# Kernel optimization log

Measured on AMD Instinct MI355X. Metric: run time of the kernel, lower is better.

The kernel has to match this reference:

```python
import jax, jax.numpy as jnp
import numpy as np

# Model constants (match init_kwargs)
H, C, OV = 6, 64, 4          # in_freq, in_dim, overlap
G, NVQ = 3, 6                # num_pvqs, num_rvqs
K, D = 1024, 8               # codebook_size, codebook_dim
FIX = H * C                  # 384
GD = (FIX * OV) // G         # 512 per product group
EPS = 1e-12


def setup_inputs() -> dict:
    key = jax.random.key(0)
    k1, k2, k3, k4 = jax.random.split(key, 4)
    B, W = 32, 2400
    z_e = jax.random.normal(k1, (B, H * W, C), dtype=jnp.float32)
    proj_down = jax.random.normal(k2, (G, D, GD), dtype=jnp.float32) * 0.05   # Linear(GD->D), torch weight layout (out,in)
    proj_up = jax.random.normal(k3, (G, GD, D), dtype=jnp.float32) * 0.05     # Linear(D->GD)
    codebooks = jax.random.normal(k4, (G, NVQ, K, D), dtype=jnp.float32)      # kaiming-normal-ish init
    return {"z_e": z_e, "proj_down": proj_down, "proj_up": proj_up,
            "codebooks": codebooks, "num_streams": 6}


def _l2norm(x):
    return x / jnp.maximum(jnp.linalg.norm(x, axis=-1, keepdims=True), EPS)


def reference(z_e, proj_down, proj_up, codebooks, num_streams):
    B = z_e.shape[0]
    W = z_e.shape[1] // H
    T = W // OV
    # pre_process: b (h w) c -> b w (c h), then fold overlap frames
    z = z_e.reshape(B, H, W, C).transpose(0, 2, 3, 1).reshape(B, W, C * H)
    z = z.reshape(B, T, OV * FIX)
    # split into G contiguous groups of GD dims -> (G, B, T, GD)
    zg = z.reshape(B, T, G, GD).transpose(2, 0, 1, 3)

    def group_fn(x, pd, pu, cbs):
        zd = jnp.einsum('btg,dg->btd', x, pd)            # proj_down: (B,T,D)
        residual = zd
        zq = jnp.zeros_like(zd)
        codes = []
        cm = jnp.float32(0.0)
        cb = jnp.float32(0.0)
        for i in range(int(num_streams)):
            en = _l2norm(cbs[i])                          # (K,D) normalized codebook
            zn = _l2norm(residual)                        # (B,T,D)
            sim = jnp.einsum('btd,kd->btk', zn, en)       # cosine sim; argmax == argmin of L2 dist
            code = jnp.argmax(sim, axis=-1)               # (B,T)
            q = en[code]                                  # gather quantized vectors
            cm = cm + jnp.mean((residual - jax.lax.stop_gradient(q)) ** 2)
            cb = cb + jnp.mean((jax.lax.stop_gradient(residual) - q) ** 2)
            q_st = residual + jax.lax.stop_gradient(q - residual)  # straight-through
            residual = residual - q_st
            zq = zq + q_st
            codes.append(code)
        idx = jnp.stack(codes, axis=1)                    # (B,NVQ,T)
        up = jnp.einsum('btd,gd->btg', zq, pu)            # proj_up: (B,T,GD)
        return up, idx, cm, cb

    up, idx, cm, cb = jax.vmap(group_fn)(zg, proj_down, proj_up, codebooks)
    # merge groups: (G,B,T,GD) -> (B,T,G*GD)
    zq = up.transpose(1, 2, 0, 3).reshape(B, T, G * GD)
    indices = idx.transpose(1, 2, 0, 3)                   # (B,NVQ,G,T)
    cm_loss = jnp.mean(cm)                                # sum over groups / num groups
    cb_loss = jnp.mean(cb)
    # post_process: unfold overlap, then b w (c h) -> b (h w) c
    zq = zq.reshape(B, T, OV, FIX).reshape(B, W, FIX)
    zq = zq.reshape(B, W, C, H).transpose(0, 3, 1, 2).reshape(B, H * W, C)
    return zq, indices, cm_loss, cb_loss
```

## Files before the change

kernel.cpp:

```cpp
#include <hip/hip_runtime.h>
#include <cfloat>
#include <math.h>

constexpr int H_  = 6;
constexpr int C_  = 64;
constexpr int OV_ = 4;
constexpr int G_  = 3;
constexpr int NVQ_ = 6;
constexpr int K_  = 1024;
constexpr int D_  = 8;
constexpr int B_  = 32;
constexpr int W_  = 2400;
constexpr int T_  = 600;
constexpr int NPOS_ = B_ * T_;
constexpr int FIX_ = H_ * C_;
constexpr int GD_ = 512;

constexpr size_t OUT_ZQ   = 0;
constexpr size_t OUT_IDX  = (size_t)B_ * H_ * W_ * C_;
constexpr size_t OUT_LOSS = OUT_IDX + (size_t)B_ * NVQ_ * G_ * T_;

constexpr size_t WS_EN   = 0;
constexpr size_t WS_ZD   = WS_EN + (size_t)G_*NVQ_*K_*D_*8;
constexpr size_t WS_LOSS = WS_ZD + (size_t)G_*NPOS_*D_*8;
constexpr size_t WS_ZQ   = WS_LOSS + 64;


__global__ __launch_bounds__(256) void k1_norm_cb(const float* __restrict__ cb,
                                                  double* __restrict__ en,
                                                  float* __restrict__ en32,
                                                  double* __restrict__ loss) {
    int tid = blockIdx.x * 256 + threadIdx.x;
    if (tid == 0) loss[0] = 0.0;
    if (tid >= G_ * NVQ_ * K_) return;
    int k  = tid & (K_ - 1);
    int gi = tid >> 10;
    const float* row = cb + ((size_t)gi * K_ + k) * D_;
    double v[D_];
    double ss = 0.0;
#pragma unroll
    for (int d = 0; d < D_; d++) { v[d] = (double)row[d]; ss += v[d] * v[d]; }
    double n = sqrt(ss);
    if (n < 1e-12) n = 1e-12;
    double* dst64 = en + ((size_t)gi * K_ + k) * D_;
    float*  dst32 = en32 + ((size_t)gi * K_ + k) * D_;
#pragma unroll
    for (int d = 0; d < D_; d++) {
        double q = v[d] / n;
        dst64[d] = q;
        dst32[d] = (float)q;
    }
}

constexpr int PSTR_ = 1548;
constexpr int OVS_  = 388;

__global__ __launch_bounds__(256) void k2_fold_pd(const float* __restrict__ ze,
                                                  const float* __restrict__ pd,
                                                  double* __restrict__ zd) {
    __shared__ __align__(16) float zf[8 * PSTR_];
    int tid  = threadIdx.x;
    int pos0 = blockIdx.x * 8;
#pragma unroll
    for (int it = 0; it < 12; it++) {
        int slot = it * 256 + tid;
        int seg  = slot >> 6;
        int li   = slot & 63;
        int p = seg / 6, h = seg - p * 6;
        int pos = pos0 + p;
        int b = pos / T_, t = pos - b * T_;
        const float4 vv = *(const float4*)(ze + ((size_t)((b * H_ + h) * W_ + 4 * t)) * C_ + li * 4);
        int ov = li >> 4;
        int c0 = (li & 15) * 4;
        int base = p * PSTR_ + ov * OVS_ + h;
        zf[base + (c0 + 0) * 6] = vv.x;
        zf[base + (c0 + 1) * 6] = vv.y;
        zf[base + (c0 + 2) * 6] = vv.z;
        zf[base + (c0 + 3) * 6] = vv.w;
    }
    __syncthreads();
    if (tid < 192) {
        int p = tid / 24;
        int combo = tid - p * 24;
        int g = combo >> 3, d = combo & 7;
        const float* pdp = pd + ((size_t)g * D_ + d) * GD_;
        int lbase = p * PSTR_;
        double acc[4] = {0.0, 0.0, 0.0, 0.0};
        for (int jj = 0; jj < GD_; jj += 16) {
#pragma unroll
            for (int u = 0; u < 4; u++) {
                int j4  = jj + u * 4;
                int gd  = g * GD_ + j4;
                int ov  = gd / FIX_;
                int rem = gd - ov * FIX_;
                float4 zv = *(const float4*)&zf[lbase + ov * OVS_ + rem];
                float4 pv = *(const float4*)&pdp[j4];
                acc[u] = fma((double)pv.x, (double)zv.x, acc[u]);
                acc[u] = fma((double)pv.y, (double)zv.y, acc[u]);
                acc[u] = fma((double)pv.z, (double)zv.z, acc[u]);
                acc[u] = fma((double)pv.w, (double)zv.w, acc[u]);
            }
        }
        zd[((size_t)g * NPOS_ + pos0 + p) * D_ + d] = (acc[0] + acc[1]) + (acc[2] + acc[3]);
    }
}

__device__ __forceinline__ void screen1(const float4 lo, const float4 hi,
                                        const float r[8], int kk,
                                        float& smax, float& s2, int& sidx) {
    float s = lo.x * r[0];
    s = fmaf(lo.y, r[1], s);
    s = fmaf(lo.z, r[2], s);
    s = fmaf(lo.w, r[3], s);
    s = fmaf(hi.x, r[4], s);
    s = fmaf(hi.y, r[5], s);
    s = fmaf(hi.z, r[6], s);
    s = fmaf(hi.w, r[7], s);
    float l = fminf(s, smax);
    s2 = fmaxf(s2, l);
    if (s > smax) { smax = s; sidx = kk; }
}

__global__ __launch_bounds__(256) void k3_rvq(const double* __restrict__ en64,
                                              const float*  __restrict__ en32,
                                              const double* __restrict__ zd,
                                              float* __restrict__ zq,
                                              double* __restrict__ loss,
                                              float* __restrict__ out_idx) {
    __shared__ float smL[2][4][64];
    __shared__ float s2L[2][4][64];
    __shared__ int   idL[2][4][64];
    int tid  = threadIdx.x;
    int lane = tid & 63;
    int wu   = __builtin_amdgcn_readfirstlane(tid >> 6);
    int g     = blockIdx.x / 300;
    int chunk = blockIdx.x - g * 300;
    int pos   = chunk * 64 + lane;
    size_t zdbase = ((size_t)g * NPOS_ + pos) * D_;

    const double* en64g = en64 + (size_t)g * NVQ_ * K_ * D_;
    const float*  en32g = en32 + (size_t)g * NVQ_ * K_ * D_;

    double r64[8]; float r32[8];
    {
        const double* zp = zd + zdbase;
#pragma unroll
        for (int d = 0; d < 8; d++) { r64[d] = zp[d]; r32[d] = (float)r64[d]; }
    }
    double loss_acc = 0.0;

    for (int i = 0; i < NVQ_; i++) {
        int p = i & 1;
        int kb = wu * 256;
        const float* cp = en32g + ((size_t)i * K_ + kb) * D_;
        float smax = -FLT_MAX, s2 = -FLT_MAX; int sidx = 0;
        for (int c = 0; c < 256; c += 8) {
            const float4* q0 = (const float4*)(cp + (size_t)(c + 0) * 8);
            const float4* q1 = (const float4*)(cp + (size_t)(c + 1) * 8);
            const float4* q2 = (const float4*)(cp + (size_t)(c + 2) * 8);
            const float4* q3 = (const float4*)(cp + (size_t)(c + 3) * 8);
            const float4* q4 = (const float4*)(cp + (size_t)(c + 4) * 8);
            const float4* q5 = (const float4*)(cp + (size_t)(c + 5) * 8);
            const float4* q6 = (const float4*)(cp + (size_t)(c + 6) * 8);
            const float4* q7 = (const float4*)(cp + (size_t)(c + 7) * 8);
            float4 a0 = q0[0], b0 = q0[1];
            float4 a1 = q1[0], b1 = q1[1];
            float4 a2 = q2[0], b2 = q2[1];
            float4 a3 = q3[0], b3 = q3[1];
            float4 a4 = q4[0], b4 = q4[1];
            float4 a5 = q5[0], b5 = q5[1];
            float4 a6 = q6[0], b6 = q6[1];
            float4 a7 = q7[0], b7 = q7[1];
            screen1(a0, b0, r32, kb + c + 0, smax, s2, sidx);
            screen1(a1, b1, r32, kb + c + 1, smax, s2, sidx);
            screen1(a2, b2, r32, kb + c + 2, smax, s2, sidx);
            screen1(a3, b3, r32, kb + c + 3, smax, s2, sidx);
            screen1(a4, b4, r32, kb + c + 4, smax, s2, sidx);
            screen1(a5, b5, r32, kb + c + 5, smax, s2, sidx);
            screen1(a6, b6, r32, kb + c + 6, smax, s2, sidx);
            screen1(a7, b7, r32, kb + c + 7, smax, s2, sidx);
        }
        smL[p][wu][lane] = smax;
        s2L[p][wu][lane] = s2;
        idL[p][wu][lane] = sidx;
        __syncthreads();
        float sm  = smL[p][0][lane];
        float s2m = s2L[p][0][lane];
        int   si  = idL[p][0][lane];
#pragma unroll
        for (int w = 1; w < 4; w++) {
            float a  = smL[p][w][lane];
            float a2 = s2L[p][w][lane];
            int   ai = idL[p][w][lane];
            float l  = fminf(a, sm);
            s2m = fmaxf(s2m, fmaxf(l, a2));
            if (a > sm) { sm = a; si = ai; }
        }
        float rr = 0.f;
#pragma unroll
        for (int d = 0; d < 8; d++) rr = fmaf(r32[d], r32[d], rr);
        float gap = sm - s2m;
        bool need = !(gap * gap > 1.6e-11f * rr);
        if (__any(need)) {
            const double* bp = en64g + (size_t)i * K_ * D_;
            double bmax = -DBL_MAX; int bidx = 0;
            for (int k = 0; k < K_; k++) {
                const double* cq = bp + (size_t)k * 8;
                double sA = cq[0] * r64[0];
                double sB = cq[1] * r64[1];
                sA = fma(cq[2], r64[2], sA);
                sB = fma(cq[3], r64[3], sB);
                sA = fma(cq[4], r64[4], sA);
                sB = fma(cq[5], r64[5], sB);
                sA = fma(cq[6], r64[6], sA);
                sB = fma(cq[7], r64[7], sB);
                double s = sA + sB;
                if (s > bmax) { bmax = s; bidx = k; }
            }
            if (need) si = bidx;
        }
        {
            const double* qp = en64g + ((size_t)i * K_ + si) * D_;
            double2 q01 = *(const double2*)(qp + 0);
            double2 q23 = *(const double2*)(qp + 2);
            double2 q45 = *(const double2*)(qp + 4);
            double2 q67 = *(const double2*)(qp + 6);
            r64[0] -= q01.x; r64[1] -= q01.y;
            r64[2] -= q23.x; r64[3] -= q23.y;
            r64[4] -= q45.x; r64[5] -= q45.y;
            r64[6] -= q67.x; r64[7] -= q67.y;
#pragma unroll
            for (int d = 0; d < 8; d++) r32[d] = (float)r64[d];
        }
        if (wu == 0) {
#pragma unroll
            for (int d = 0; d < 8; d++) loss_acc = fma(r64[d], r64[d], loss_acc);
            int b = pos / T_, t = pos - b * T_;
            out_idx[((size_t)(b * NVQ_ + i) * G_ + g) * T_ + t] = (float)si;
        }
    }
    if (wu == 0) {
        const double* zp = zd + zdbase;
        float4 o0, o1;
        o0.x = (float)(zp[0] - r64[0]);
        o0.y = (float)(zp[1] - r64[1]);
        o0.z = (float)(zp[2] - r64[2]);
        o0.w = (float)(zp[3] - r64[3]);
        o1.x = (float)(zp[4] - r64[4]);
        o1.y = (float)(zp[5] - r64[5]);
        o1.z = (float)(zp[6] - r64[6]);
        o1.w = (float)(zp[7] - r64[7]);
        *(float4*)(zq + zdbase)     = o0;
        *(float4*)(zq + zdbase + 4) = o1;
#pragma unroll
        for (int off = 32; off >= 1; off >>= 1) loss_acc += __shfl_xor(loss_acc, off);
        if (lane == 0) atomicAdd(loss, loss_acc);
    }
}

__global__ __launch_bounds__(512) void k4_up(const float* __restrict__ zq,
                                             const float* __restrict__ pu,
                                             const double* __restrict__ loss,
                                             float* __restrict__ out_zq,
                                             float* __restrict__ out_loss) {
    __shared__ __align__(16) float pu_s[G_ * GD_ * 9];
    int tid = threadIdx.x;
#pragma unroll
    for (int it = 0; it < 3; it++) {
        int row = it * 512 + tid;
        float4 lo = *(const float4*)(pu + (size_t)row * 8);
        float4 hi = *(const float4*)(pu + (size_t)row * 8 + 4);
        float* dst = &pu_s[row * 9];
        dst[0] = lo.x; dst[1] = lo.y; dst[2] = lo.z; dst[3] = lo.w;
        dst[4] = hi.x; dst[5] = hi.y; dst[6] = hi.z; dst[7] = hi.w;
    }
    if (blockIdx.x == 0 && tid == 0) {
        double l = loss[0] * (1.0 / 460800.0);
        out_loss[0] = (float)l;
        out_loss[1] = (float)l;
    }
    __syncthreads();
    int wv = tid >> 6, lane = tid & 63;
    int pos = blockIdx.x * 8 + wv;
    int b = pos / T_, t = pos - b * T_;
    int ov = lane >> 4, c0 = (lane & 15) * 4;
    int gd_min = ov * FIX_ + c0 * 6;
    int g_lo = gd_min >> 9;
    int g_hi = g_lo < 2 ? g_lo + 1 : 2;
    float za[8], zb[8];
    const float* zqa = zq + ((size_t)g_lo * NPOS_ + pos) * D_;
    const float* zqb = zq + ((size_t)g_hi * NPOS_ + pos) * D_;
#pragma unroll
    for (int d = 0; d < 8; d++) { za[d] = zqa[d]; zb[d] = zqb[d]; }
#pragma unroll
    for (int h = 0; h < H_; h++) {
        float4 o;
        float* op = &o.x;
#pragma unroll
        for (int q = 0; q < 4; q++) {
            int gd = ov * FIX_ + (c0 + q) * 6 + h;
            int g  = gd >> 9;
            int j  = gd & 511;
            const float* pr = &pu_s[(g * GD_ + j) * 9];
            bool hi = (g != g_lo);
            float acc = 0.f;
#pragma unroll
            for (int d = 0; d < 8; d++) {
                float zv = hi ? zb[d] : za[d];
                acc = fmaf(zv, pr[d], acc);
            }
            op[q] = acc;
        }
        *(float4*)(out_zq + ((size_t)((b * H_ + h) * W_ + 4 * t + ov)) * C_ + c0) = o;
    }
}

extern "C" void kernel_launch(void* const* d_in, const int* in_sizes, int n_in,
                              void* d_out, int out_size, void* d_ws, size_t ws_size,
                              hipStream_t stream) {
    const float* ze = (const float*)d_in[0];
    const float* pd = (const float*)d_in[1];
    const float* pu = (const float*)d_in[2];
    const float* cb = (const float*)d_in[3];

    float* out = (float*)d_out;
    char*  ws  = (char*)d_ws;
    double* ws_en   = (double*)(ws + WS_EN);
    double* ws_zd   = (double*)(ws + WS_ZD);
    double* ws_loss = (double*)(ws + WS_LOSS);
    float*  ws_zq   = (float*)(ws + WS_ZQ);
    float* en32 = out + OUT_ZQ;

    k1_norm_cb<<<(G_ * NVQ_ * K_ + 255) / 256, 256, 0, stream>>>(cb, ws_en, en32, ws_loss);
    k2_fold_pd<<<NPOS_ / 8, 256, 0, stream>>>(ze, pd, ws_zd);
    k3_rvq<<<G_ * (NPOS_ / 64), 256, 0, stream>>>(ws_en, en32, ws_zd, ws_zq, ws_loss, out + OUT_IDX);
    k4_up<<<NPOS_ / 8, 512, 0, stream>>>(ws_zq, pu, ws_loss, out + OUT_ZQ, out + OUT_LOSS);
}
```

Measured before the change: 630.1 us.

## Split RVQ codebook scan across 8 waves and swizzle proj_up LDS layout

The RVQ kernel now runs 512 threads per block, so eight waves each screen 128 codewords instead of four waves each screening 256. The cross-wave argmax reduction widens to match. This is meant to shorten each block's serial scan and raise occupancy, at the cost of more shared-memory reduction traffic and possible register pressure under the new launch bounds. Separately, the up-projection kernel replaces its padded 9-float LDS rows with dense 8-float rows using an XOR swizzle, so each weight row can be read as two float4 vector loads while avoiding bank conflicts.

```diff
diff --git a/kernel.cpp b/kernel.cpp
--- a/kernel.cpp
+++ b/kernel.cpp
@@ -121,15 +121,15 @@
     if (s > smax) { smax = s; sidx = kk; }
 }
 
-__global__ __launch_bounds__(256) void k3_rvq(const double* __restrict__ en64,
-                                              const float*  __restrict__ en32,
-                                              const double* __restrict__ zd,
-                                              float* __restrict__ zq,
-                                              double* __restrict__ loss,
-                                              float* __restrict__ out_idx) {
-    __shared__ float smL[2][4][64];
-    __shared__ float s2L[2][4][64];
-    __shared__ int   idL[2][4][64];
+__global__ __launch_bounds__(512, 4) void k3_rvq(const double* __restrict__ en64,
+                                                 const float*  __restrict__ en32,
+                                                 const double* __restrict__ zd,
+                                                 float* __restrict__ zq,
+                                                 double* __restrict__ loss,
+                                                 float* __restrict__ out_idx) {
+    __shared__ float smL[2][8][64];
+    __shared__ float s2L[2][8][64];
+    __shared__ int   idL[2][8][64];
     int tid  = threadIdx.x;
     int lane = tid & 63;
     int wu   = __builtin_amdgcn_readfirstlane(tid >> 6);
@@ -151,10 +151,10 @@
 
     for (int i = 0; i < NVQ_; i++) {
         int p = i & 1;
-        int kb = wu * 256;
+        int kb = wu * 128;
         const float* cp = en32g + ((size_t)i * K_ + kb) * D_;
         float smax = -FLT_MAX, s2 = -FLT_MAX; int sidx = 0;
-        for (int c = 0; c < 256; c += 8) {
+        for (int c = 0; c < 128; c += 8) {
             const float4* q0 = (const float4*)(cp + (size_t)(c + 0) * 8);
             const float4* q1 = (const float4*)(cp + (size_t)(c + 1) * 8);
             const float4* q2 = (const float4*)(cp + (size_t)(c + 2) * 8);
@@ -188,7 +188,7 @@
         float s2m = s2L[p][0][lane];
         int   si  = idL[p][0][lane];
 #pragma unroll
-        for (int w = 1; w < 4; w++) {
+        for (int w = 1; w < 8; w++) {
             float a  = smL[p][w][lane];
             float a2 = s2L[p][w][lane];
             int   ai = idL[p][w][lane];
@@ -258,21 +258,26 @@
     }
 }
 
+__device__ __forceinline__ int swz48(int byte) {
+    return byte ^ (((byte >> 8) & 7) << 4);
+}
+
 __global__ __launch_bounds__(512) void k4_up(const float* __restrict__ zq,
                                              const float* __restrict__ pu,
                                              const double* __restrict__ loss,
                                              float* __restrict__ out_zq,
                                              float* __restrict__ out_loss) {
-    __shared__ __align__(16) float pu_s[G_ * GD_ * 9];
+    __shared__ __align__(16) float pu_s[G_ * GD_ * 8];
+    char* pb = (char*)pu_s;
     int tid = threadIdx.x;
 #pragma unroll
     for (int it = 0; it < 3; it++) {
         int row = it * 512 + tid;
         float4 lo = *(const float4*)(pu + (size_t)row * 8);
         float4 hi = *(const float4*)(pu + (size_t)row * 8 + 4);
-        float* dst = &pu_s[row * 9];
-        dst[0] = lo.x; dst[1] = lo.y; dst[2] = lo.z; dst[3] = lo.w;
-        dst[4] = hi.x; dst[5] = hi.y; dst[6] = hi.z; dst[7] = hi.w;
+        int byte0 = row * 32;
+        *(float4*)(pb + swz48(byte0))      = lo;
+        *(float4*)(pb + swz48(byte0 + 16)) = hi;
     }
     if (blockIdx.x == 0 && tid == 0) {
         double l = loss[0] * (1.0 / 460800.0);
@@ -299,16 +304,19 @@
 #pragma unroll
         for (int q = 0; q < 4; q++) {
             int gd = ov * FIX_ + (c0 + q) * 6 + h;
-            int g  = gd >> 9;
-            int j  = gd & 511;
-            const float* pr = &pu_s[(g * GD_ + j) * 9];
-            bool hi = (g != g_lo);
-            float acc = 0.f;
-#pragma unroll
-            for (int d = 0; d < 8; d++) {
-                float zv = hi ? zb[d] : za[d];
-                acc = fmaf(zv, pr[d], acc);
-            }
+            int byte0 = gd * 32;
+            float4 fa = *(const float4*)(pb + swz48(byte0));
+            float4 fb = *(const float4*)(pb + swz48(byte0 + 16));
+            bool hi = ((gd >> 9) != g_lo);
+            const float* zv = hi ? zb : za;
+            float acc = zv[0] * fa.x;
+            acc = fmaf(zv[1], fa.y, acc);
+            acc = fmaf(zv[2], fa.z, acc);
+            acc = fmaf(zv[3], fa.w, acc);
+            acc = fmaf(zv[4], fb.x, acc);
+            acc = fmaf(zv[5], fb.y, acc);
+            acc = fmaf(zv[6], fb.z, acc);
+            acc = fmaf(zv[7], fb.w, acc);
             op[q] = acc;
         }
         *(float4*)(out_zq + ((size_t)((b * H_ + h) * W_ + 4 * t + ov)) * C_ + c0) = o;
@@ -333,6 +341,6 @@
 
     k1_norm_cb<<<(G_ * NVQ_ * K_ + 255) / 256, 256, 0, stream>>>(cb, ws_en, en32, ws_loss);
     k2_fold_pd<<<NPOS_ / 8, 256, 0, stream>>>(ze, pd, ws_zd);
-    k3_rvq<<<G_ * (NPOS_ / 64), 256, 0, stream>>>(ws_en, en32, ws_zd, ws_zq, ws_loss, out + OUT_IDX);
+    k3_rvq<<<G_ * (NPOS_ / 64), 512, 0, stream>>>(ws_en, en32, ws_zd, ws_zq, ws_loss, out + OUT_IDX);
     k4_up<<<NPOS_ / 8, 512, 0, stream>>>(ws_zq, pu, ws_loss, out + OUT_ZQ, out + OUT_LOSS);
 }
```

Result: faster. 581.1 us (-7.8%).
